# Performance work log

Measured on AMD Instinct MI355X. Metric: run time of the kernel, lower is better.

Reference implementation:

```python
import jax, jax.numpy as jnp
import numpy as np
import math

B, S, D, H = 4, 2048, 1024, 16
DH = D // H  # per-head dim = 64
MASK_VAL = -1000000.0


def setup_inputs() -> dict:
    key = jax.random.key(0)
    ks = jax.random.split(key, 9)
    queries = jax.random.normal(ks[0], (B, S, D), dtype=jnp.float32)
    keys = jax.random.normal(ks[1], (B, S, D), dtype=jnp.float32)
    values = jax.random.normal(ks[2], (B, S, D), dtype=jnp.float32)
    valid_lens = jax.random.randint(ks[3], (B,), 0, S, dtype=jnp.int32)
    scale = 1.0 / math.sqrt(D)
    Wq = jax.random.normal(ks[4], (D, D), dtype=jnp.float32) * scale
    Wk = jax.random.normal(ks[5], (D, D), dtype=jnp.float32) * scale
    Wv = jax.random.normal(ks[6], (D, D), dtype=jnp.float32) * scale
    Wo = jax.random.normal(ks[7], (D, D), dtype=jnp.float32) * scale
    return {"queries": queries, "keys": keys, "values": values,
            "valid_lens": valid_lens, "Wq": Wq, "Wk": Wk, "Wv": Wv, "Wo": Wo}


def _split_heads(x):  # [B,S,D] -> [B,H,S,DH]
    b, s, _ = x.shape
    return x.reshape(b, s, H, DH).transpose(0, 2, 1, 3)


def reference(queries, keys, values, valid_lens, Wq, Wk, Wv, Wo):
    q = _split_heads(queries @ Wq)  # [B,H,S,DH]
    k = _split_heads(keys @ Wk)
    v = _split_heads(values @ Wv)
    scores = jnp.einsum('bhqd,bhkd->bhqk', q, k) / jnp.sqrt(jnp.float32(DH))
    # mask key positions >= valid_len[b] (sequence_mask with value=-1e6)
    key_pos = jnp.arange(S)  # [S]
    mask = key_pos[None, None, None, :] < valid_lens[:, None, None, None]  # [B,1,1,S]
    scores = jnp.where(mask, scores, MASK_VAL)
    attn = jax.nn.softmax(scores, axis=-1)  # [B,H,S,S] -- the 1GB intermediate
    out = jnp.einsum('bhqk,bhkd->bhqd', attn, v)  # [B,H,S,DH]
    out = out.transpose(0, 2, 1, 3).reshape(B, S, D)  # concat heads
    return out @ Wo
```

## Files before the change

### kernel.cpp

```cpp
#include <hip/hip_runtime.h>

#define BB 4
#define SS 2048
#define DD 1024
#define HH 16
#define DHH 64

typedef _Float16 half8 __attribute__((ext_vector_type(8)));
typedef _Float16 half4v __attribute__((ext_vector_type(4)));
typedef _Float16 half2v __attribute__((ext_vector_type(2)));
typedef float floatx4 __attribute__((ext_vector_type(4)));

#define GLOBAL_AS __attribute__((address_space(1)))
#define LDS_AS __attribute__((address_space(3)))

#define QSCALE 0.18033688011112042f

__global__ void wt_kernel(const float* __restrict__ w0, const float* __restrict__ w1,
                          const float* __restrict__ w2, const float* __restrict__ w3,
                          _Float16* __restrict__ wt) {
  __shared__ float tile[32][33];
  int z = blockIdx.z;
  const float* w = (z == 0) ? w0 : (z == 1) ? w1 : (z == 2) ? w2 : w3;
  _Float16* dst = wt + (size_t)z * 1024 * 1024;
  int k0 = blockIdx.x * 32, n0 = blockIdx.y * 32;
  int tx = threadIdx.x & 31, ty = threadIdx.x >> 5;
#pragma unroll
  for (int r = ty; r < 32; r += 8) tile[r][tx] = w[(size_t)(k0 + r) * 1024 + n0 + tx];
  __syncthreads();
#pragma unroll
  for (int r = ty; r < 32; r += 8) dst[(size_t)(n0 + r) * 1024 + k0 + tx] = (_Float16)tile[tx][r];
}

__global__ __launch_bounds__(256) void qkv_gemm(const float* __restrict__ Qin,
                                                const float* __restrict__ Kin,
                                                const float* __restrict__ Vin,
                                                const _Float16* __restrict__ Wt,
                                                _Float16* __restrict__ Qf,
                                                _Float16* __restrict__ Kf,
                                                _Float16* __restrict__ Vt) {
  __shared__ _Float16 lA[128 * 32];
  __shared__ _Float16 lB[128 * 32];
  int tid = threadIdx.x;
  int wave = tid >> 6, lane = tid & 63, quad = lane >> 4, l15 = lane & 15;
  int wgid = blockIdx.y * 8 + blockIdx.x;
  int swz = (wgid & 7) * 192 + (wgid >> 3);
  int bn = swz & 7, bm = swz >> 3;
  int proj = bm >> 6;
  int wm = wave >> 1, wn = wave & 1;

  const float* src = (proj == 0) ? Qin : (proj == 1) ? Kin : Vin;
  const float* A = src + (size_t)(bm & 63) * 128 * 1024;
  const _Float16* W = Wt + (size_t)proj * 1024 * 1024;

  floatx4 fzero = {0.f, 0.f, 0.f, 0.f};
  floatx4 acc[4][4];
#pragma unroll
  for (int i = 0; i < 4; ++i)
#pragma unroll
    for (int j = 0; j < 4; ++j) acc[i][j] = fzero;

  int g0 = tid, g1 = 256 + tid;
  int row0 = g0 >> 2, gc0 = (g0 & 3) ^ ((row0 >> 1) & 3);
  int row1 = g1 >> 2, gc1 = (g1 & 3) ^ ((row1 >> 1) & 3);
  const float* a0 = A + ((size_t)row0 * 1024 + gc0 * 8);
  const float* a1 = A + ((size_t)row1 * 1024 + gc1 * 8);
  const _Float16* b0 = W + ((size_t)(bn * 128 + row0) * 1024 + gc0 * 8);
  const _Float16* b1 = W + ((size_t)(bn * 128 + row1) * 1024 + gc1 * 8);

  for (int k0 = 0; k0 < 1024; k0 += 32) {
    __builtin_amdgcn_global_load_lds((const GLOBAL_AS void*)(b0 + k0),
                                     (LDS_AS void*)(lB + g0 * 8), 16, 0, 0);
    __builtin_amdgcn_global_load_lds((const GLOBAL_AS void*)(b1 + k0),
                                     (LDS_AS void*)(lB + g1 * 8), 16, 0, 0);
    float4 fa0 = *(const float4*)(a0 + k0);
    float4 fa1 = *(const float4*)(a0 + k0 + 4);
    float4 fa2 = *(const float4*)(a1 + k0);
    float4 fa3 = *(const float4*)(a1 + k0 + 4);
    half8 ha0 = {(_Float16)fa0.x, (_Float16)fa0.y, (_Float16)fa0.z, (_Float16)fa0.w,
                 (_Float16)fa1.x, (_Float16)fa1.y, (_Float16)fa1.z, (_Float16)fa1.w};
    half8 ha1 = {(_Float16)fa2.x, (_Float16)fa2.y, (_Float16)fa2.z, (_Float16)fa2.w,
                 (_Float16)fa3.x, (_Float16)fa3.y, (_Float16)fa3.z, (_Float16)fa3.w};
    *(half8*)(lA + g0 * 8) = ha0;
    *(half8*)(lA + g1 * 8) = ha1;
    __syncthreads();

    half8 af[4], bf[4];
#pragma unroll
    for (int i = 0; i < 4; ++i) {
      int row = wm * 64 + i * 16 + l15;
      af[i] = *(const half8*)(lA + (row * 4 + (quad ^ ((row >> 1) & 3))) * 8);
    }
#pragma unroll
    for (int j = 0; j < 4; ++j) {
      int row = wn * 64 + j * 16 + l15;
      bf[j] = *(const half8*)(lB + (row * 4 + (quad ^ ((row >> 1) & 3))) * 8);
    }
#pragma unroll
    for (int i = 0; i < 4; ++i)
#pragma unroll
      for (int j = 0; j < 4; ++j)
        acc[i][j] = __builtin_amdgcn_mfma_f32_16x16x32_f16(af[i], bf[j], acc[i][j], 0, 0, 0);
    __syncthreads();
  }

  int rloc = (bm & 63) * 128;
#pragma unroll
  for (int i = 0; i < 4; ++i) {
#pragma unroll
    for (int j = 0; j < 4; ++j) {
      int rowb = rloc + wm * 64 + i * 16 + quad * 4;
      int col = bn * 128 + wn * 64 + j * 16 + l15;
      if (proj == 0) {
#pragma unroll
        for (int r = 0; r < 4; ++r)
          Qf[(size_t)(rowb + r) * 1024 + col] = (_Float16)(acc[i][j][r] * QSCALE);
      } else if (proj == 1) {
#pragma unroll
        for (int r = 0; r < 4; ++r)
          Kf[(size_t)(rowb + r) * 1024 + col] = (_Float16)acc[i][j][r];
      } else {
        int b = rowb >> 11, s = rowb & 2047;
        half4v pk = {(_Float16)acc[i][j][0], (_Float16)acc[i][j][1],
                     (_Float16)acc[i][j][2], (_Float16)acc[i][j][3]};
        *(half4v*)(Vt + (size_t)(b * 1024 + col) * 2048 + s) = pk;
      }
    }
  }
}

__global__ __launch_bounds__(256) void gemm_out(const _Float16* __restrict__ A,
                                                const _Float16* __restrict__ Wt,
                                                float* __restrict__ C) {
  __shared__ _Float16 lA[128 * 32];
  __shared__ _Float16 lB[128 * 32];
  int tid = threadIdx.x;
  int wave = tid >> 6, lane = tid & 63, quad = lane >> 4, l15 = lane & 15;
  int wgid = blockIdx.y * 8 + blockIdx.x;
  int swz = (wgid & 7) * 64 + (wgid >> 3);
  int bn = swz & 7, bm = swz >> 3;
  int wm = wave >> 1, wn = wave & 1;

  floatx4 fzero = {0.f, 0.f, 0.f, 0.f};
  floatx4 acc[4][4];
#pragma unroll
  for (int i = 0; i < 4; ++i)
#pragma unroll
    for (int j = 0; j < 4; ++j) acc[i][j] = fzero;

  int g0 = tid, g1 = 256 + tid;
  int row0 = g0 >> 2, gc0 = (g0 & 3) ^ ((row0 >> 1) & 3);
  int row1 = g1 >> 2, gc1 = (g1 & 3) ^ ((row1 >> 1) & 3);
  const _Float16* a0 = A + ((size_t)(bm * 128 + row0) * 1024 + gc0 * 8);
  const _Float16* a1 = A + ((size_t)(bm * 128 + row1) * 1024 + gc1 * 8);
  const _Float16* b0 = Wt + ((size_t)(bn * 128 + row0) * 1024 + gc0 * 8);
  const _Float16* b1 = Wt + ((size_t)(bn * 128 + row1) * 1024 + gc1 * 8);

  for (int k0 = 0; k0 < 1024; k0 += 32) {
    __builtin_amdgcn_global_load_lds((const GLOBAL_AS void*)(a0 + k0),
                                     (LDS_AS void*)(lA + g0 * 8), 16, 0, 0);
    __builtin_amdgcn_global_load_lds((const GLOBAL_AS void*)(a1 + k0),
                                     (LDS_AS void*)(lA + g1 * 8), 16, 0, 0);
    __builtin_amdgcn_global_load_lds((const GLOBAL_AS void*)(b0 + k0),
                                     (LDS_AS void*)(lB + g0 * 8), 16, 0, 0);
    __builtin_amdgcn_global_load_lds((const GLOBAL_AS void*)(b1 + k0),
                                     (LDS_AS void*)(lB + g1 * 8), 16, 0, 0);
    __syncthreads();

    half8 af[4], bf[4];
#pragma unroll
    for (int i = 0; i < 4; ++i) {
      int row = wm * 64 + i * 16 + l15;
      af[i] = *(const half8*)(lA + (row * 4 + (quad ^ ((row >> 1) & 3))) * 8);
    }
#pragma unroll
    for (int j = 0; j < 4; ++j) {
      int row = wn * 64 + j * 16 + l15;
      bf[j] = *(const half8*)(lB + (row * 4 + (quad ^ ((row >> 1) & 3))) * 8);
    }
#pragma unroll
    for (int i = 0; i < 4; ++i)
#pragma unroll
      for (int j = 0; j < 4; ++j)
        acc[i][j] = __builtin_amdgcn_mfma_f32_16x16x32_f16(af[i], bf[j], acc[i][j], 0, 0, 0);
    __syncthreads();
  }

#pragma unroll
  for (int i = 0; i < 4; ++i)
#pragma unroll
    for (int j = 0; j < 4; ++j) {
      int rowb = bm * 128 + wm * 64 + i * 16 + quad * 4;
      int col = bn * 128 + wn * 64 + j * 16 + l15;
#pragma unroll
      for (int r = 0; r < 4; ++r) C[(size_t)(rowb + r) * 1024 + col] = acc[i][j][r];
    }
}

__global__ __launch_bounds__(256) void attn_kernel(const _Float16* __restrict__ Q,
                                                   const _Float16* __restrict__ K,
                                                   const _Float16* __restrict__ Vt,
                                                   const int* __restrict__ vlens,
                                                   _Float16* __restrict__ O) {
  __shared__ _Float16 lK[2][64 * 64];
  __shared__ _Float16 lV[2][64 * 64];
  __shared__ _Float16 lP[4 * 16 * 64];

  int tid = threadIdx.x, wave = tid >> 6, lane = tid & 63, quad = lane >> 4, l15 = lane & 15;
  int bh = blockIdx.y, b = bh >> 4, h = bh & 15;
  int q0 = blockIdx.x * 64;
  int vlen = vlens[b];
  int nch = (vlen == 0) ? (SS / 64) : ((vlen + 63) >> 6);
  float mask_val = (vlen == 0) ? 0.0f : -1.0e6f;

  const _Float16* qb = Q + ((size_t)(b * SS + q0 + wave * 16 + l15) * DD + h * 64 + quad * 8);
  half8 qf0 = *(const half8*)qb;
  half8 qf1 = *(const half8*)(qb + 32);

  int ss0 = tid, ss1 = tid + 256;
  int srow0 = ss0 >> 3, sgc0 = ss0 & 7;
  int srow1 = ss1 >> 3, sgc1 = ss1 & 7;
  int sidx0 = (srow0 * 8 + (sgc0 ^ (srow0 & 7))) * 8;
  int sidx1 = (srow1 * 8 + (sgc1 ^ (srow1 & 7))) * 8;
  const _Float16* kp0 = K + ((size_t)(b * SS + srow0) * DD + h * 64 + sgc0 * 8);
  const _Float16* kp1 = K + ((size_t)(b * SS + srow1) * DD + h * 64 + sgc1 * 8);
  const _Float16* vp0 = Vt + ((size_t)(b * DD + h * 64 + srow0) * SS + sgc0 * 8);
  const _Float16* vp1 = Vt + ((size_t)(b * DD + h * 64 + srow1) * SS + sgc1 * 8);

  int off[2][4];
#pragma unroll
  for (int ks = 0; ks < 2; ++ks)
#pragma unroll
    for (int j = 0; j < 4; ++j) {
      int row = j * 16 + l15, gc = ks * 4 + quad;
      off[ks][j] = (row * 8 + (gc ^ (row & 7))) * 8;
    }
  int pbase = wave * 1024 + l15 * 64;
  int wp[4], rpl[2], rph[2];
#pragma unroll
  for (int j = 0; j < 4; ++j) wp[j] = pbase + (((j * 4 + quad) ^ l15) << 2);
#pragma unroll
  for (int ks = 0; ks < 2; ++ks) {
    int gl = ks * 8 + quad * 2;
    rpl[ks] = pbase + ((gl ^ l15) << 2);
    rph[ks] = pbase + (((gl + 1) ^ l15) << 2);
  }

  float l_acc = 0.f;
  floatx4 fzero = {0.f, 0.f, 0.f, 0.f};
  floatx4 o[4];
#pragma unroll
  for (int j = 0; j < 4; ++j) o[j] = fzero;

  half8 rk0 = *(const half8*)kp0;
  half8 rk1 = *(const half8*)kp1;
  half8 rv0 = *(const half8*)vp0;
  half8 rv1 = *(const half8*)vp1;
  *(half8*)(lK[0] + sidx0) = rk0;
  *(half8*)(lK[0] + sidx1) = rk1;
  *(half8*)(lV[0] + sidx0) = rv0;
  *(half8*)(lV[0] + sidx1) = rv1;
  int cur = 0;

  for (int kc = 0; kc < nch; ++kc) {
    __syncthreads();

    int kn = (kc + 1 < nch) ? kc + 1 : kc;
    size_t koff = (size_t)kn * 64 * DD;
    size_t voff = (size_t)kn * 64;
    rk0 = *(const half8*)(kp0 + koff);
    rk1 = *(const half8*)(kp1 + koff);
    rv0 = *(const half8*)(vp0 + voff);
    rv1 = *(const half8*)(vp1 + voff);

    const _Float16* cK = lK[cur];
    const _Float16* cV = lV[cur];
    int kb = kc * 64;

    floatx4 sacc[4];
#pragma unroll
    for (int j = 0; j < 4; ++j) sacc[j] = fzero;
    __builtin_amdgcn_s_setprio(1);
#pragma unroll
    for (int ks = 0; ks < 2; ++ks) {
      half8 qf = ks ? qf1 : qf0;
#pragma unroll
      for (int j = 0; j < 4; ++j) {
        half8 kf = *(const half8*)(cK + off[ks][j]);
        sacc[j] = __builtin_amdgcn_mfma_f32_16x16x32_f16(kf, qf, sacc[j], 0, 0, 0);
      }
    }
    __builtin_amdgcn_s_setprio(0);

    float p[4][4];
    if (kb + 64 <= vlen) {
#pragma unroll
      for (int j = 0; j < 4; ++j)
#pragma unroll
        for (int r = 0; r < 4; ++r) p[j][r] = __builtin_amdgcn_exp2f(sacc[j][r]);
    } else {
#pragma unroll
      for (int j = 0; j < 4; ++j)
#pragma unroll
        for (int r = 0; r < 4; ++r) {
          int key = kb + j * 16 + quad * 4 + r;
          float s = (key < vlen) ? sacc[j][r] : mask_val;
          p[j][r] = __builtin_amdgcn_exp2f(s);
        }
    }

#pragma unroll
    for (int j = 0; j < 4; ++j) {
      l_acc += (p[j][0] + p[j][1]) + (p[j][2] + p[j][3]);
      half2v lo = __builtin_bit_cast(half2v, __builtin_amdgcn_cvt_pkrtz(p[j][0], p[j][1]));
      half2v hi = __builtin_bit_cast(half2v, __builtin_amdgcn_cvt_pkrtz(p[j][2], p[j][3]));
      half4v w4 = {lo.x, lo.y, hi.x, hi.y};
      *(half4v*)(lP + wp[j]) = w4;
    }

    __builtin_amdgcn_s_setprio(1);
#pragma unroll
    for (int ks = 0; ks < 2; ++ks) {
      half4v plo = *(const half4v*)(lP + rpl[ks]);
      half4v phi = *(const half4v*)(lP + rph[ks]);
      half8 pf = {plo.x, plo.y, plo.z, plo.w, phi.x, phi.y, phi.z, phi.w};
#pragma unroll
      for (int j = 0; j < 4; ++j) {
        half8 vf = *(const half8*)(cV + off[ks][j]);
        o[j] = __builtin_amdgcn_mfma_f32_16x16x32_f16(pf, vf, o[j], 0, 0, 0);
      }
    }
    __builtin_amdgcn_s_setprio(0);

    _Float16* nK = lK[cur ^ 1];
    _Float16* nV = lV[cur ^ 1];
    *(half8*)(nK + sidx0) = rk0;
    *(half8*)(nK + sidx1) = rk1;
    *(half8*)(nV + sidx0) = rv0;
    *(half8*)(nV + sidx1) = rv1;
    cur ^= 1;
  }

  float l = l_acc;
  l += __shfl_xor(l, 16);
  l += __shfl_xor(l, 32);
  float inv = 1.0f / l;
  float inv_r[4];
#pragma unroll
  for (int r = 0; r < 4; ++r) inv_r[r] = __shfl(inv, quad * 4 + r);
#pragma unroll
  for (int j = 0; j < 4; ++j) {
    int col = h * 64 + j * 16 + l15;
#pragma unroll
    for (int r = 0; r < 4; ++r) {
      int qrow = q0 + wave * 16 + quad * 4 + r;
      O[(size_t)(b * SS + qrow) * DD + col] = (_Float16)(o[j][r] * inv_r[r]);
    }
  }
}

extern "C" void kernel_launch(void* const* d_in, const int* in_sizes, int n_in,
                              void* d_out, int out_size, void* d_ws, size_t ws_size,
                              hipStream_t stream) {
  const float* q = (const float*)d_in[0];
  const float* k = (const float*)d_in[1];
  const float* v = (const float*)d_in[2];
  const int* vl = (const int*)d_in[3];
  const float* wq = (const float*)d_in[4];
  const float* wk = (const float*)d_in[5];
  const float* wv = (const float*)d_in[6];
  const float* wo = (const float*)d_in[7];

  char* ws = (char*)d_ws;
  _Float16* Wt = (_Float16*)ws;
  _Float16* Of = (_Float16*)(ws + (8u << 20));
  _Float16* Qf = (_Float16*)(ws + (56u << 20));
  _Float16* Kf = (_Float16*)(ws + (72u << 20));
  _Float16* Vt = (_Float16*)(ws + (88u << 20));

  dim3 blk(256);

  wt_kernel<<<dim3(32, 32, 4), blk, 0, stream>>>(wq, wk, wv, wo, Wt);
  qkv_gemm<<<dim3(8, 192), blk, 0, stream>>>(q, k, v, Wt, Qf, Kf, Vt);
  attn_kernel<<<dim3(32, 64), blk, 0, stream>>>(Qf, Kf, Vt, vl, Of);
  gemm_out<<<dim3(8, 64), blk, 0, stream>>>(Of, Wt + (3u << 20), (float*)d_out);
}
```

Baseline: 336.1 us.

## Double-buffer LDS tiles in QKV and output projection GEMMs

```diff
diff --git a/kernel.cpp b/kernel.cpp
--- a/kernel.cpp
+++ b/kernel.cpp
@@ -39,8 +39,8 @@
                                                 _Float16* __restrict__ Qf,
                                                 _Float16* __restrict__ Kf,
                                                 _Float16* __restrict__ Vt) {
-  __shared__ _Float16 lA[128 * 32];
-  __shared__ _Float16 lB[128 * 32];
+  __shared__ _Float16 lA[2][128 * 32];
+  __shared__ _Float16 lB[2][128 * 32];
   int tid = threadIdx.x;
   int wave = tid >> 6, lane = tid & 63, quad = lane >> 4, l15 = lane & 15;
   int wgid = blockIdx.y * 8 + blockIdx.x;
@@ -68,40 +68,71 @@
   const _Float16* b0 = W + ((size_t)(bn * 128 + row0) * 1024 + gc0 * 8);
   const _Float16* b1 = W + ((size_t)(bn * 128 + row1) * 1024 + gc1 * 8);
 
+  int aoff[4], boff[4];
+#pragma unroll
+  for (int i = 0; i < 4; ++i) {
+    int row = wm * 64 + i * 16 + l15;
+    aoff[i] = (row * 4 + (quad ^ ((row >> 1) & 3))) * 8;
+  }
+#pragma unroll
+  for (int j = 0; j < 4; ++j) {
+    int row = wn * 64 + j * 16 + l15;
+    boff[j] = (row * 4 + (quad ^ ((row >> 1) & 3))) * 8;
+  }
+
+  __builtin_amdgcn_global_load_lds((const GLOBAL_AS void*)b0,
+                                   (LDS_AS void*)(lB[0] + g0 * 8), 16, 0, 0);
+  __builtin_amdgcn_global_load_lds((const GLOBAL_AS void*)b1,
+                                   (LDS_AS void*)(lB[0] + g1 * 8), 16, 0, 0);
+  {
+    float4 fa0 = *(const float4*)a0;
+    float4 fa1 = *(const float4*)(a0 + 4);
+    float4 fa2 = *(const float4*)a1;
+    float4 fa3 = *(const float4*)(a1 + 4);
+    half8 h0 = {(_Float16)fa0.x, (_Float16)fa0.y, (_Float16)fa0.z, (_Float16)fa0.w,
+                (_Float16)fa1.x, (_Float16)fa1.y, (_Float16)fa1.z, (_Float16)fa1.w};
+    half8 h1 = {(_Float16)fa2.x, (_Float16)fa2.y, (_Float16)fa2.z, (_Float16)fa2.w,
+                (_Float16)fa3.x, (_Float16)fa3.y, (_Float16)fa3.z, (_Float16)fa3.w};
+    *(half8*)(lA[0] + g0 * 8) = h0;
+    *(half8*)(lA[0] + g1 * 8) = h1;
+  }
+  int cur = 0;
+
   for (int k0 = 0; k0 < 1024; k0 += 32) {
-    __builtin_amdgcn_global_load_lds((const GLOBAL_AS void*)(b0 + k0),
-                                     (LDS_AS void*)(lB + g0 * 8), 16, 0, 0);
-    __builtin_amdgcn_global_load_lds((const GLOBAL_AS void*)(b1 + k0),
-                                     (LDS_AS void*)(lB + g1 * 8), 16, 0, 0);
-    float4 fa0 = *(const float4*)(a0 + k0);
-    float4 fa1 = *(const float4*)(a0 + k0 + 4);
-    float4 fa2 = *(const float4*)(a1 + k0);
-    float4 fa3 = *(const float4*)(a1 + k0 + 4);
-    half8 ha0 = {(_Float16)fa0.x, (_Float16)fa0.y, (_Float16)fa0.z, (_Float16)fa0.w,
-                 (_Float16)fa1.x, (_Float16)fa1.y, (_Float16)fa1.z, (_Float16)fa1.w};
-    half8 ha1 = {(_Float16)fa2.x, (_Float16)fa2.y, (_Float16)fa2.z, (_Float16)fa2.w,
-                 (_Float16)fa3.x, (_Float16)fa3.y, (_Float16)fa3.z, (_Float16)fa3.w};
-    *(half8*)(lA + g0 * 8) = ha0;
-    *(half8*)(lA + g1 * 8) = ha1;
     __syncthreads();
 
+    int kn = (k0 + 32 < 1024) ? (k0 + 32) : k0;
+    if (kn != k0) {
+      __builtin_amdgcn_global_load_lds((const GLOBAL_AS void*)(b0 + kn),
+                                       (LDS_AS void*)(lB[cur ^ 1] + g0 * 8), 16, 0, 0);
+      __builtin_amdgcn_global_load_lds((const GLOBAL_AS void*)(b1 + kn),
+                                       (LDS_AS void*)(lB[cur ^ 1] + g1 * 8), 16, 0, 0);
+    }
+    float4 na0 = *(const float4*)(a0 + kn);
+    float4 na1 = *(const float4*)(a0 + kn + 4);
+    float4 na2 = *(const float4*)(a1 + kn);
+    float4 na3 = *(const float4*)(a1 + kn + 4);
+
+    const _Float16* cA = lA[cur];
+    const _Float16* cB = lB[cur];
     half8 af[4], bf[4];
 #pragma unroll
-    for (int i = 0; i < 4; ++i) {
-      int row = wm * 64 + i * 16 + l15;
-      af[i] = *(const half8*)(lA + (row * 4 + (quad ^ ((row >> 1) & 3))) * 8);
-    }
-#pragma unroll
-    for (int j = 0; j < 4; ++j) {
-      int row = wn * 64 + j * 16 + l15;
-      bf[j] = *(const half8*)(lB + (row * 4 + (quad ^ ((row >> 1) & 3))) * 8);
-    }
+    for (int i = 0; i < 4; ++i) af[i] = *(const half8*)(cA + aoff[i]);
+#pragma unroll
+    for (int j = 0; j < 4; ++j) bf[j] = *(const half8*)(cB + boff[j]);
 #pragma unroll
     for (int i = 0; i < 4; ++i)
 #pragma unroll
       for (int j = 0; j < 4; ++j)
         acc[i][j] = __builtin_amdgcn_mfma_f32_16x16x32_f16(af[i], bf[j], acc[i][j], 0, 0, 0);
-    __syncthreads();
+
+    half8 h0 = {(_Float16)na0.x, (_Float16)na0.y, (_Float16)na0.z, (_Float16)na0.w,
+                (_Float16)na1.x, (_Float16)na1.y, (_Float16)na1.z, (_Float16)na1.w};
+    half8 h1 = {(_Float16)na2.x, (_Float16)na2.y, (_Float16)na2.z, (_Float16)na2.w,
+                (_Float16)na3.x, (_Float16)na3.y, (_Float16)na3.z, (_Float16)na3.w};
+    *(half8*)(lA[cur ^ 1] + g0 * 8) = h0;
+    *(half8*)(lA[cur ^ 1] + g1 * 8) = h1;
+    cur ^= 1;
   }
 
   int rloc = (bm & 63) * 128;
@@ -132,8 +163,8 @@
 __global__ __launch_bounds__(256) void gemm_out(const _Float16* __restrict__ A,
                                                 const _Float16* __restrict__ Wt,
                                                 float* __restrict__ C) {
-  __shared__ _Float16 lA[128 * 32];
-  __shared__ _Float16 lB[128 * 32];
+  __shared__ _Float16 lA[2][128 * 32];
+  __shared__ _Float16 lB[2][128 * 32];
   int tid = threadIdx.x;
   int wave = tid >> 6, lane = tid & 63, quad = lane >> 4, l15 = lane & 15;
   int wgid = blockIdx.y * 8 + blockIdx.x;
@@ -156,34 +187,54 @@
   const _Float16* b0 = Wt + ((size_t)(bn * 128 + row0) * 1024 + gc0 * 8);
   const _Float16* b1 = Wt + ((size_t)(bn * 128 + row1) * 1024 + gc1 * 8);
 
+  int aoff[4], boff[4];
+#pragma unroll
+  for (int i = 0; i < 4; ++i) {
+    int row = wm * 64 + i * 16 + l15;
+    aoff[i] = (row * 4 + (quad ^ ((row >> 1) & 3))) * 8;
+  }
+#pragma unroll
+  for (int j = 0; j < 4; ++j) {
+    int row = wn * 64 + j * 16 + l15;
+    boff[j] = (row * 4 + (quad ^ ((row >> 1) & 3))) * 8;
+  }
+
+  __builtin_amdgcn_global_load_lds((const GLOBAL_AS void*)a0,
+                                   (LDS_AS void*)(lA[0] + g0 * 8), 16, 0, 0);
+  __builtin_amdgcn_global_load_lds((const GLOBAL_AS void*)a1,
+                                   (LDS_AS void*)(lA[0] + g1 * 8), 16, 0, 0);
+  __builtin_amdgcn_global_load_lds((const GLOBAL_AS void*)b0,
+                                   (LDS_AS void*)(lB[0] + g0 * 8), 16, 0, 0);
+  __builtin_amdgcn_global_load_lds((const GLOBAL_AS void*)b1,
+                                   (LDS_AS void*)(lB[0] + g1 * 8), 16, 0, 0);
+  int cur = 0;
+
   for (int k0 = 0; k0 < 1024; k0 += 32) {
-    __builtin_amdgcn_global_load_lds((const GLOBAL_AS void*)(a0 + k0),
-                                     (LDS_AS void*)(lA + g0 * 8), 16, 0, 0);
-    __builtin_amdgcn_global_load_lds((const GLOBAL_AS void*)(a1 + k0),
-                                     (LDS_AS void*)(lA + g1 * 8), 16, 0, 0);
-    __builtin_amdgcn_global_load_lds((const GLOBAL_AS void*)(b0 + k0),
-                                     (LDS_AS void*)(lB + g0 * 8), 16, 0, 0);
-    __builtin_amdgcn_global_load_lds((const GLOBAL_AS void*)(b1 + k0),
-                                     (LDS_AS void*)(lB + g1 * 8), 16, 0, 0);
     __syncthreads();
-
+    if (k0 + 32 < 1024) {
+      __builtin_amdgcn_global_load_lds((const GLOBAL_AS void*)(a0 + k0 + 32),
+                                       (LDS_AS void*)(lA[cur ^ 1] + g0 * 8), 16, 0, 0);
+      __builtin_amdgcn_global_load_lds((const GLOBAL_AS void*)(a1 + k0 + 32),
+                                       (LDS_AS void*)(lA[cur ^ 1] + g1 * 8), 16, 0, 0);
+      __builtin_amdgcn_global_load_lds((const GLOBAL_AS void*)(b0 + k0 + 32),
+                                       (LDS_AS void*)(lB[cur ^ 1] + g0 * 8), 16, 0, 0);
+      __builtin_amdgcn_global_load_lds((const GLOBAL_AS void*)(b1 + k0 + 32),
+                                       (LDS_AS void*)(lB[cur ^ 1] + g1 * 8), 16, 0, 0);
+    }
+
+    const _Float16* cA = lA[cur];
+    const _Float16* cB = lB[cur];
     half8 af[4], bf[4];
 #pragma unroll
-    for (int i = 0; i < 4; ++i) {
-      int row = wm * 64 + i * 16 + l15;
-      af[i] = *(const half8*)(lA + (row * 4 + (quad ^ ((row >> 1) & 3))) * 8);
-    }
-#pragma unroll
-    for (int j = 0; j < 4; ++j) {
-      int row = wn * 64 + j * 16 + l15;
-      bf[j] = *(const half8*)(lB + (row * 4 + (quad ^ ((row >> 1) & 3))) * 8);
-    }
+    for (int i = 0; i < 4; ++i) af[i] = *(const half8*)(cA + aoff[i]);
+#pragma unroll
+    for (int j = 0; j < 4; ++j) bf[j] = *(const half8*)(cB + boff[j]);
 #pragma unroll
     for (int i = 0; i < 4; ++i)
 #pragma unroll
       for (int j = 0; j < 4; ++j)
         acc[i][j] = __builtin_amdgcn_mfma_f32_16x16x32_f16(af[i], bf[j], acc[i][j], 0, 0, 0);
-    __syncthreads();
+    cur ^= 1;
   }
 
 #pragma unroll
```

Result: faster. 324.5 us (-3.5%).
